# Optimization experiments

Hardware: AMD Instinct MI355X
Metric: run time of the kernel (lower is better)

Reference implementation:

```python
import jax, jax.numpy as jnp
import numpy as np

WIN = 9
PAD = WIN // 2    # floor(9/2) = 4
WIN_SIZE = WIN * WIN
EPS = 1e-05


def _box_sum(x):
    # 9x9 ones-kernel conv, stride 1, pad 4 (SAME size), NCHW with C=1
    filt = jnp.ones((1, 1, WIN, WIN), dtype=x.dtype)
    return jax.lax.conv_general_dilated(
        x, filt, window_strides=(1, 1),
        padding=[(PAD, PAD), (PAD, PAD)],
        dimension_numbers=('NCHW', 'OIHW', 'NCHW'))


def setup_inputs() -> dict:
    key = jax.random.key(0)
    k1, k2 = jax.random.split(key)
    I = jax.random.normal(k1, (8, 1, 1024, 1024), dtype=jnp.float32)
    J = jax.random.normal(k2, (8, 1, 1024, 1024), dtype=jnp.float32)
    return {"I": I, "J": J}


def reference(I, J):
    I_sum = _box_sum(I)
    J_sum = _box_sum(J)
    I2_sum = _box_sum(I * I)
    J2_sum = _box_sum(J * J)
    IJ_sum = _box_sum(I * J)

    u_I = I_sum / WIN_SIZE
    u_J = J_sum / WIN_SIZE

    cross = IJ_sum - u_J * I_sum - u_I * J_sum + u_I * u_J * WIN_SIZE
    I_var = I2_sum - 2 * u_I * I_sum + u_I * u_I * WIN_SIZE
    J_var = J2_sum - 2 * u_J * J_sum + u_J * u_J * WIN_SIZE

    cc = cross * cross / (I_var * J_var + EPS)
    return jnp.mean(cc)
```

## Files before the change

### kernel.cpp

```cpp
#include <hip/hip_runtime.h>

#define H 1024
#define W 1024
#define NIMG 8
#define TX 64
#define CY 8
#define NBX (W / TX)
#define NBY (H / CY)
#define NBLOCKS (NBX * NBY * NIMG)
#define EPS 1e-5f

__device__ __forceinline__ void load16(const float* __restrict__ Ip,
                                       const float* __restrict__ Jp,
                                       int y, int xbase, bool xfast,
                                       float* __restrict__ a,
                                       float* __restrict__ b) {
  if (y >= 0 && y < H) {
    const float* Irow = Ip + (size_t)y * W;
    const float* Jrow = Jp + (size_t)y * W;
    if (xfast) {
      const float4* pa = reinterpret_cast<const float4*>(Irow + xbase);
      const float4* pb = reinterpret_cast<const float4*>(Jrow + xbase);
      #pragma unroll
      for (int q = 0; q < 4; ++q) {
        float4 va = pa[q], vb = pb[q];
        a[4*q+0]=va.x; a[4*q+1]=va.y; a[4*q+2]=va.z; a[4*q+3]=va.w;
        b[4*q+0]=vb.x; b[4*q+1]=vb.y; b[4*q+2]=vb.z; b[4*q+3]=vb.w;
      }
    } else {
      #pragma unroll
      for (int k = 0; k < 16; ++k) {
        int xx = xbase + k;
        bool in = (xx >= 0) && (xx < W);
        a[k] = in ? Irow[xx] : 0.0f;
        b[k] = in ? Jrow[xx] : 0.0f;
      }
    }
  } else {
    #pragma unroll
    for (int k = 0; k < 16; ++k) { a[k] = 0.0f; b[k] = 0.0f; }
  }
}

__device__ __forceinline__ void rowsum8(const float* __restrict__ a,
                                        const float* __restrict__ b,
                                        int r, int xg,
                                        float4 (*rs4)[TX], float (*rs1)[TX]) {
  float sI=0.f, sJ=0.f, sII=0.f, sJJ=0.f, sIJ=0.f;
  #pragma unroll
  for (int k = 0; k < 9; ++k) {
    sI  += a[k];        sJ  += b[k];
    sII += a[k]*a[k];   sJJ += b[k]*b[k];
    sIJ += a[k]*b[k];
  }
  const int xg8 = xg * 8;
  #pragma unroll
  for (int i = 0; i < 8; ++i) {
    if (i > 0) {
      float an=a[i+8], al=a[i-1], bn=b[i+8], bl=b[i-1];
      sI  += an - al;         sJ  += bn - bl;
      sII += an*an - al*al;   sJJ += bn*bn - bl*bl;
      sIJ += an*bn - al*bl;
    }
    const int px = xg8 + (i ^ xg);
    rs4[r][px] = make_float4(sI, sJ, sII, sJJ);
    rs1[r][px] = sIJ;
  }
}

__global__ __launch_bounds__(64, 2)
void ncc_main(const float* __restrict__ I, const float* __restrict__ J,
              float* __restrict__ partial) {
  __shared__ float4 rs4[16][TX];
  __shared__ float  rs1[16][TX];

  const int tid = threadIdx.x;
  const int gx = blockIdx.x, gy = blockIdx.y, n = blockIdx.z;
  const size_t img_off = (size_t)n * H * W;
  const float* Ip = I + img_off;
  const float* Jp = J + img_off;

  const int rb = tid >> 3;
  const int xg = tid & 7;
  const int xbase = gx * TX + xg * 8 - 4;
  const bool xfast = (xbase >= 0) && (xbase + 16 <= W);
  const int ybase = gy * CY - 4;

  float a0[16], b0[16], a1[16], b1[16];
  load16(Ip, Jp, ybase + rb,     xbase, xfast, a0, b0);
  load16(Ip, Jp, ybase + rb + 8, xbase, xfast, a1, b1);
  rowsum8(a0, b0, rb,     xg, rs4, rs1);
  rowsum8(a1, b1, rb + 8, xg, rs4, rs1);
  __syncthreads();

  const int x  = tid;
  const int xs = (x & ~7) | ((x ^ (x >> 3)) & 7);
  float4 h4[16]; float h1[16];
  #pragma unroll
  for (int k = 0; k < 16; ++k) { h4[k] = rs4[k][xs]; h1[k] = rs1[k][xs]; }

  float wI=0.f, wJ=0.f, wII=0.f, wJJ=0.f, wIJ=0.f;
  #pragma unroll
  for (int k = 0; k < 9; ++k) {
    wI += h4[k].x; wJ += h4[k].y; wII += h4[k].z; wJJ += h4[k].w;
    wIJ += h1[k];
  }
  const float inv81 = 1.0f / 81.0f;
  float acc = 0.f;
  #pragma unroll
  for (int i = 0; i < 8; ++i) {
    if (i > 0) {
      wI  += h4[8+i].x - h4[i-1].x;  wJ  += h4[8+i].y - h4[i-1].y;
      wII += h4[8+i].z - h4[i-1].z;  wJJ += h4[8+i].w - h4[i-1].w;
      wIJ += h1[8+i]   - h1[i-1];
    }
    float cross = fmaf(-(wI * wJ), inv81, wIJ);
    float Iv    = fmaf(-(wI * wI), inv81, wII);
    float Jv    = fmaf(-(wJ * wJ), inv81, wJJ);
    acc = fmaf(cross * cross,
               __builtin_amdgcn_rcpf(fmaf(Iv, Jv, EPS)), acc);
  }

  #pragma unroll
  for (int off = 32; off > 0; off >>= 1)
    acc += __shfl_down(acc, off, 64);
  if (tid == 0) {
    const int blin = blockIdx.x + NBX * (blockIdx.y + NBY * (int)blockIdx.z);
    partial[blin] = acc;
  }
}

__global__ __launch_bounds__(256)
void ncc_reduce(const float* __restrict__ partial, float* __restrict__ out) {
  __shared__ float red[4];
  const int tid = threadIdx.x;
  const float4* p4 = reinterpret_cast<const float4*>(partial);
  float s = 0.f;
  #pragma unroll 4
  for (int i = tid; i < NBLOCKS / 4; i += 256) {
    float4 v = p4[i];
    s += (v.x + v.y) + (v.z + v.w);
  }
  #pragma unroll
  for (int off = 32; off > 0; off >>= 1)
    s += __shfl_down(s, off, 64);
  if ((tid & 63) == 0) red[tid >> 6] = s;
  __syncthreads();
  if (tid == 0)
    out[0] = (red[0] + red[1] + red[2] + red[3]) *
             (1.0f / (float)((size_t)NIMG * H * W));
}

extern "C" void kernel_launch(void* const* d_in, const int* in_sizes, int n_in,
                              void* d_out, int out_size, void* d_ws, size_t ws_size,
                              hipStream_t stream) {
  const float* I = (const float*)d_in[0];
  const float* J = (const float*)d_in[1];
  float* out     = (float*)d_out;
  float* partial = (float*)d_ws;

  dim3 grid(NBX, NBY, NIMG);
  hipLaunchKernelGGL(ncc_main, grid, dim3(64), 0, stream, I, J, partial);
  hipLaunchKernelGGL(ncc_reduce, dim3(1), dim3(256), 0, stream, partial, out);
}
```

Baseline: 119.9 us.

## Replace shared-memory 2D box sums with per-thread vertical sliding window over rows

Each thread now owns 4 columns and walks a strip of 16 output rows, keeping running vertical window sums in registers. It adds each new row's horizontal sums and subtracts the row leaving the window, instead of staging row sums in LDS and recomputing a 16-row halo per 8-row tile. This removes LDS traffic, the barrier, and much of the redundant halo reads. In exchange there are fewer, larger blocks with a longer serial row loop. Each row is still loaded twice (add and subtract), relying on cache, and sliding-window cancellation may cost a little float accuracy.

```diff
diff --git a/kernel.cpp b/kernel.cpp
--- a/kernel.cpp
+++ b/kernel.cpp
@@ -3,130 +3,117 @@
 #define H 1024
 #define W 1024
 #define NIMG 8
-#define TX 64
-#define CY 8
-#define NBX (W / TX)
-#define NBY (H / CY)
-#define NBLOCKS (NBX * NBY * NIMG)
+#define CPT 4
+#define TH 16
+#define NBX 4
+#define WPB 4
+#define NBY (H / (TH * WPB))
+#define NWAVES (NBX * NBY * NIMG * WPB)
 #define EPS 1e-5f
 
-__device__ __forceinline__ void load16(const float* __restrict__ Ip,
-                                       const float* __restrict__ Jp,
-                                       int y, int xbase, bool xfast,
-                                       float* __restrict__ a,
-                                       float* __restrict__ b) {
-  if (y >= 0 && y < H) {
-    const float* Irow = Ip + (size_t)y * W;
-    const float* Jrow = Jp + (size_t)y * W;
-    if (xfast) {
-      const float4* pa = reinterpret_cast<const float4*>(Irow + xbase);
-      const float4* pb = reinterpret_cast<const float4*>(Jrow + xbase);
-      #pragma unroll
-      for (int q = 0; q < 4; ++q) {
-        float4 va = pa[q], vb = pb[q];
-        a[4*q+0]=va.x; a[4*q+1]=va.y; a[4*q+2]=va.z; a[4*q+3]=va.w;
-        b[4*q+0]=vb.x; b[4*q+1]=vb.y; b[4*q+2]=vb.z; b[4*q+3]=vb.w;
-      }
-    } else {
-      #pragma unroll
-      for (int k = 0; k < 16; ++k) {
-        int xx = xbase + k;
-        bool in = (xx >= 0) && (xx < W);
-        a[k] = in ? Irow[xx] : 0.0f;
-        b[k] = in ? Jrow[xx] : 0.0f;
-      }
-    }
-  } else {
-    #pragma unroll
-    for (int k = 0; k < 16; ++k) { a[k] = 0.0f; b[k] = 0.0f; }
+struct RS { float I[CPT], J[CPT], II[CPT], JJ[CPT], IJ[CPT]; };
+
+__device__ __forceinline__ void row_rs(const float* __restrict__ Irow,
+                                       const float* __restrict__ Jrow,
+                                       int X, bool okL, bool okR, RS& o) {
+  float a[12], b[12];
+  { float4 q = *reinterpret_cast<const float4*>(Irow + X);
+    a[4]=q.x; a[5]=q.y; a[6]=q.z; a[7]=q.w;
+    float4 p = *reinterpret_cast<const float4*>(Jrow + X);
+    b[4]=p.x; b[5]=p.y; b[6]=p.z; b[7]=p.w; }
+  if (okL) {
+    float4 q = *reinterpret_cast<const float4*>(Irow + X - 4);
+    a[0]=q.x; a[1]=q.y; a[2]=q.z; a[3]=q.w;
+    float4 p = *reinterpret_cast<const float4*>(Jrow + X - 4);
+    b[0]=p.x; b[1]=p.y; b[2]=p.z; b[3]=p.w;
+  } else { a[0]=a[1]=a[2]=a[3]=0.f; b[0]=b[1]=b[2]=b[3]=0.f; }
+  if (okR) {
+    float4 q = *reinterpret_cast<const float4*>(Irow + X + 4);
+    a[8]=q.x; a[9]=q.y; a[10]=q.z; a[11]=q.w;
+    float4 p = *reinterpret_cast<const float4*>(Jrow + X + 4);
+    b[8]=p.x; b[9]=p.y; b[10]=p.z; b[11]=p.w;
+  } else { a[8]=a[9]=a[10]=a[11]=0.f; b[8]=b[9]=b[10]=b[11]=0.f; }
+
+  float sI=0.f, sJ=0.f, sII=0.f, sJJ=0.f, sIJ=0.f;
+  #pragma unroll
+  for (int k = 0; k < 9; ++k) {
+    sI += a[k]; sJ += b[k];
+    sII = fmaf(a[k], a[k], sII);
+    sJJ = fmaf(b[k], b[k], sJJ);
+    sIJ = fmaf(a[k], b[k], sIJ);
+  }
+  o.I[0]=sI; o.J[0]=sJ; o.II[0]=sII; o.JJ[0]=sJJ; o.IJ[0]=sIJ;
+  #pragma unroll
+  for (int i = 1; i < CPT; ++i) {
+    float an=a[i+8], al=a[i-1], bn=b[i+8], bl=b[i-1];
+    sI += an - al;  sJ += bn - bl;
+    sII = fmaf(-al, al, fmaf(an, an, sII));
+    sJJ = fmaf(-bl, bl, fmaf(bn, bn, sJJ));
+    sIJ = fmaf(-al, bl, fmaf(an, bn, sIJ));
+    o.I[i]=sI; o.J[i]=sJ; o.II[i]=sII; o.JJ[i]=sJJ; o.IJ[i]=sIJ;
   }
 }
 
-__device__ __forceinline__ void rowsum8(const float* __restrict__ a,
-                                        const float* __restrict__ b,
-                                        int r, int xg,
-                                        float4 (*rs4)[TX], float (*rs1)[TX]) {
-  float sI=0.f, sJ=0.f, sII=0.f, sJJ=0.f, sIJ=0.f;
-  #pragma unroll
-  for (int k = 0; k < 9; ++k) {
-    sI  += a[k];        sJ  += b[k];
-    sII += a[k]*a[k];   sJJ += b[k]*b[k];
-    sIJ += a[k]*b[k];
-  }
-  const int xg8 = xg * 8;
-  #pragma unroll
-  for (int i = 0; i < 8; ++i) {
-    if (i > 0) {
-      float an=a[i+8], al=a[i-1], bn=b[i+8], bl=b[i-1];
-      sI  += an - al;         sJ  += bn - bl;
-      sII += an*an - al*al;   sJJ += bn*bn - bl*bl;
-      sIJ += an*bn - al*bl;
-    }
-    const int px = xg8 + (i ^ xg);
-    rs4[r][px] = make_float4(sI, sJ, sII, sJJ);
-    rs1[r][px] = sIJ;
-  }
-}
-
-__global__ __launch_bounds__(64, 2)
+__global__ __launch_bounds__(256, 2)
 void ncc_main(const float* __restrict__ I, const float* __restrict__ J,
               float* __restrict__ partial) {
-  __shared__ float4 rs4[16][TX];
-  __shared__ float  rs1[16][TX];
-
-  const int tid = threadIdx.x;
-  const int gx = blockIdx.x, gy = blockIdx.y, n = blockIdx.z;
-  const size_t img_off = (size_t)n * H * W;
+  const int tid  = threadIdx.x;
+  const int lane = tid & 63, wv = tid >> 6;
+  const int X  = blockIdx.x * 256 + lane * CPT;
+  const int y0 = (blockIdx.y * WPB + wv) * TH;
+  const bool okL = (X >= 4);
+  const bool okR = (X + 8 <= W);
+  const size_t img_off = (size_t)blockIdx.z * H * W;
   const float* Ip = I + img_off;
   const float* Jp = J + img_off;
 
-  const int rb = tid >> 3;
-  const int xg = tid & 7;
-  const int xbase = gx * TX + xg * 8 - 4;
-  const bool xfast = (xbase >= 0) && (xbase + 16 <= W);
-  const int ybase = gy * CY - 4;
+  float wI[CPT], wJ[CPT], wII[CPT], wJJ[CPT], wIJ[CPT];
+  #pragma unroll
+  for (int i = 0; i < CPT; ++i) { wI[i]=wJ[i]=wII[i]=wJJ[i]=wIJ[i]=0.f; }
+  float acc = 0.f;
+  const float inv81 = 1.0f / 81.0f;
 
-  float a0[16], b0[16], a1[16], b1[16];
-  load16(Ip, Jp, ybase + rb,     xbase, xfast, a0, b0);
-  load16(Ip, Jp, ybase + rb + 8, xbase, xfast, a1, b1);
-  rowsum8(a0, b0, rb,     xg, rs4, rs1);
-  rowsum8(a1, b1, rb + 8, xg, rs4, rs1);
-  __syncthreads();
+  auto apply = [&](int r, float sgn) {
+    if ((unsigned)r < (unsigned)H) {
+      RS o;
+      row_rs(Ip + (size_t)r * W, Jp + (size_t)r * W, X, okL, okR, o);
+      #pragma unroll
+      for (int i = 0; i < CPT; ++i) {
+        wI[i]  = fmaf(sgn, o.I[i],  wI[i]);
+        wJ[i]  = fmaf(sgn, o.J[i],  wJ[i]);
+        wII[i] = fmaf(sgn, o.II[i], wII[i]);
+        wJJ[i] = fmaf(sgn, o.JJ[i], wJJ[i]);
+        wIJ[i] = fmaf(sgn, o.IJ[i], wIJ[i]);
+      }
+    }
+  };
+  auto emit = [&]() {
+    #pragma unroll
+    for (int i = 0; i < CPT; ++i) {
+      float cross = fmaf(-(wI[i] * wJ[i]), inv81, wIJ[i]);
+      float Iv    = fmaf(-(wI[i] * wI[i]), inv81, wII[i]);
+      float Jv    = fmaf(-(wJ[i] * wJ[i]), inv81, wJJ[i]);
+      acc = fmaf(cross * cross,
+                 __builtin_amdgcn_rcpf(fmaf(Iv, Jv, EPS)), acc);
+    }
+  };
 
-  const int x  = tid;
-  const int xs = (x & ~7) | ((x ^ (x >> 3)) & 7);
-  float4 h4[16]; float h1[16];
-  #pragma unroll
-  for (int k = 0; k < 16; ++k) { h4[k] = rs4[k][xs]; h1[k] = rs1[k][xs]; }
-
-  float wI=0.f, wJ=0.f, wII=0.f, wJJ=0.f, wIJ=0.f;
-  #pragma unroll
-  for (int k = 0; k < 9; ++k) {
-    wI += h4[k].x; wJ += h4[k].y; wII += h4[k].z; wJJ += h4[k].w;
-    wIJ += h1[k];
-  }
-  const float inv81 = 1.0f / 81.0f;
-  float acc = 0.f;
-  #pragma unroll
-  for (int i = 0; i < 8; ++i) {
-    if (i > 0) {
-      wI  += h4[8+i].x - h4[i-1].x;  wJ  += h4[8+i].y - h4[i-1].y;
-      wII += h4[8+i].z - h4[i-1].z;  wJJ += h4[8+i].w - h4[i-1].w;
-      wIJ += h1[8+i]   - h1[i-1];
-    }
-    float cross = fmaf(-(wI * wJ), inv81, wIJ);
-    float Iv    = fmaf(-(wI * wI), inv81, wII);
-    float Jv    = fmaf(-(wJ * wJ), inv81, wJJ);
-    acc = fmaf(cross * cross,
-               __builtin_amdgcn_rcpf(fmaf(Iv, Jv, EPS)), acc);
+  for (int k = 0; k < 8; ++k) apply(y0 - 4 + k, 1.0f);
+  apply(y0 + 4, 1.0f);
+  emit();
+  for (int k = 0; k < TH - 1; ++k) {
+    apply(y0 + 5 + k, 1.0f);
+    apply(y0 - 4 + k, -1.0f);
+    emit();
   }
 
   #pragma unroll
   for (int off = 32; off > 0; off >>= 1)
     acc += __shfl_down(acc, off, 64);
-  if (tid == 0) {
-    const int blin = blockIdx.x + NBX * (blockIdx.y + NBY * (int)blockIdx.z);
-    partial[blin] = acc;
+  if (lane == 0) {
+    const int wid = (((int)blockIdx.z * NBY + (int)blockIdx.y) * NBX
+                     + (int)blockIdx.x) * WPB + wv;
+    partial[wid] = acc;
   }
 }
 
@@ -136,8 +123,8 @@
   const int tid = threadIdx.x;
   const float4* p4 = reinterpret_cast<const float4*>(partial);
   float s = 0.f;
-  #pragma unroll 4
-  for (int i = tid; i < NBLOCKS / 4; i += 256) {
+  #pragma unroll
+  for (int i = tid; i < NWAVES / 4; i += 256) {
     float4 v = p4[i];
     s += (v.x + v.y) + (v.z + v.w);
   }
@@ -160,6 +147,6 @@
   float* partial = (float*)d_ws;
 
   dim3 grid(NBX, NBY, NIMG);
-  hipLaunchKernelGGL(ncc_main, grid, dim3(64), 0, stream, I, J, partial);
+  hipLaunchKernelGGL(ncc_main, grid, dim3(256), 0, stream, I, J, partial);
   hipLaunchKernelGGL(ncc_reduce, dim3(1), dim3(256), 0, stream, partial, out);
 }
```

New measurement: 111.0 us. -7.5%, faster.
